# Optimization experiments

Hardware: AMD Instinct MI355X
Metric: run time of the kernel (lower is better)

Reference implementation:

```python
import jax, jax.numpy as jnp
import numpy as np

EPS_BN = 1e-5


def gcn_agg(h, src, dst, n):
    # remove_self_loops then add_self_loops, degree computed on dst (incl. self loops)
    valid = (src != dst).astype(h.dtype)  # mask out original self loops
    deg = jnp.zeros((n,), h.dtype).at[dst].add(valid) + 1.0  # +1 for added self loop
    dinv = deg ** -0.5
    w = dinv[src] * dinv[dst] * valid  # [E]
    # h_prime[dst] += w * h[src]; self-loop contributes deg^-1 * h
    out = jnp.zeros_like(h).at[dst].add(w[:, None] * h[src])
    out = out + (1.0 / deg)[:, None] * h
    return out


def batchnorm(h):
    # BatchNorm1d(affine=False, track_running_stats=False): batch stats, biased var
    mean = jnp.mean(h, axis=0)
    var = jnp.var(h, axis=0)
    return (h - mean) * jax.lax.rsqrt(var + EPS_BN)


def setup_inputs() -> dict:
    key = jax.random.key(0)
    ks = jax.random.split(key, 8)
    N, E, IN, HID, OUT = 50000, 640000, 500, 128, 64
    x = jax.random.normal(ks[0], (N, IN), jnp.float32)
    edge_index = jax.random.randint(ks[1], (2, E), 0, N, jnp.int64)
    def xavier(k, shape):
        gain = 1.414
        bound = gain * np.sqrt(6.0 / (shape[0] + shape[1]))
        return jax.random.uniform(k, shape, jnp.float32, -bound, bound)
    W0 = xavier(ks[2], (HID, IN))
    W1 = xavier(ks[3], (HID, HID))
    W2 = xavier(ks[4], (OUT, HID))
    b0 = jnp.zeros((HID,), jnp.float32)
    b1 = jnp.zeros((HID,), jnp.float32)
    b2 = jnp.zeros((OUT,), jnp.float32)
    return {"x": x, "edge_index": edge_index, "W0": W0, "b0": b0,
            "W1": W1, "b1": b1, "W2": W2, "b2": b2}


def reference(x, edge_index, W0, b0, W1, b1, W2, b2):
    n = x.shape[0]
    src, dst = edge_index[0], edge_index[1]
    # layer 0 and 1 (num_layers - 1 = 2), eval mode -> dropout is identity
    h = x @ W0.T
    h = gcn_agg(h, src, dst, n) + b0
    h = jax.nn.relu(batchnorm(h))
    h = h @ W1.T
    h = gcn_agg(h, src, dst, n) + b1
    h = jax.nn.relu(batchnorm(h))
    # classifier
    h = h @ W2.T
    h = gcn_agg(h, src, dst, n) + b2
    return jax.nn.log_softmax(h, axis=1)
```

## Files before the change

kernel.cpp:

```cpp
#include <hip/hip_runtime.h>
#include <hip/hip_bf16.h>
#include <math.h>


#define EPS_BN 1e-5f

typedef __attribute__((ext_vector_type(8))) _Float16 f16x8;
typedef __attribute__((ext_vector_type(4))) _Float16 f16x4;
typedef __attribute__((ext_vector_type(2))) _Float16 f16x2;
typedef __attribute__((ext_vector_type(4))) float    f32x4;

__device__ __forceinline__ void gload16(const void* g, void* l) {
    __builtin_amdgcn_global_load_lds(
        (const __attribute__((address_space(1))) void*)g,
        (__attribute__((address_space(3))) void*)l, 16, 0, 0);
}


__global__ void countw_k(const int* __restrict__ src, const int* __restrict__ dst,
                         int* __restrict__ cnt, int E, int gE,
                         const float* __restrict__ W0, _Float16* __restrict__ W0h,
                         const float* __restrict__ W1, _Float16* __restrict__ W1h,
                         const float* __restrict__ W2, _Float16* __restrict__ W2h) {
    if (blockIdx.x < (unsigned)gE) {
        int e = blockIdx.x * 256 + threadIdx.x;
        if (e >= E) return;
        int s = src[e], d = dst[e];
        if (s != d) atomicAdd(&cnt[d], 1);
        return;
    }
    int idx = (blockIdx.x - gE) * 256 + threadIdx.x;
    if (idx < 16384) {
        int r = idx >> 7, k4 = (idx & 127) * 4;
        f16x4 h = {(_Float16)0.f, (_Float16)0.f, (_Float16)0.f, (_Float16)0.f};
        if (k4 < 500) {
            float4 v = *(const float4*)(W0 + (size_t)r * 500 + k4);
            h[0] = (_Float16)v.x; h[1] = (_Float16)v.y;
            h[2] = (_Float16)v.z; h[3] = (_Float16)v.w;
        }
        *(f16x4*)(W0h + (size_t)r * 512 + k4) = h;
    } else if (idx < 16384 + 4096) {
        int t = idx - 16384;
        float4 v = *(const float4*)(W1 + (size_t)t * 4);
        f16x4 h;
        h[0] = (_Float16)v.x; h[1] = (_Float16)v.y;
        h[2] = (_Float16)v.z; h[3] = (_Float16)v.w;
        *(f16x4*)(W1h + (size_t)t * 4) = h;
    } else if (idx < 22528) {
        int t = idx - 20480;
        float4 v = *(const float4*)(W2 + (size_t)t * 4);
        f16x4 h;
        h[0] = (_Float16)v.x; h[1] = (_Float16)v.y;
        h[2] = (_Float16)v.z; h[3] = (_Float16)v.w;
        *(f16x4*)(W2h + (size_t)t * 4) = h;
    }
}

__global__ void scan1_k(const int* __restrict__ cnt, int* __restrict__ within,
                        int* __restrict__ btot, int n) {
    __shared__ int s[512];
    int tid = threadIdx.x;
    int i = blockIdx.x * 512 + tid;
    int val = (i < n) ? cnt[i] : 0;
    s[tid] = val;
    __syncthreads();
    for (int off = 1; off < 512; off <<= 1) {
        int v = (tid >= off) ? s[tid - off] : 0;
        __syncthreads();
        s[tid] += v;
        __syncthreads();
    }
    if (i < n) within[i] = s[tid] - val;
    if (tid == 511) btot[blockIdx.x] = s[511];
}

__global__ void scan3_k(const int* __restrict__ within, const int* __restrict__ btot,
                        const int* __restrict__ cnt, int* __restrict__ row_start,
                        int* __restrict__ cursor, float* __restrict__ dinv,
                        float* __restrict__ invdeg, int n) {
    __shared__ int sred[256];
    const int tid = threadIdx.x;
    const int w = (blockIdx.x * 256) >> 9;
    sred[tid] = (tid < w) ? btot[tid] : 0;
    __syncthreads();
    #pragma unroll
    for (int off = 128; off >= 1; off >>= 1) {
        if (tid < off) sred[tid] += sred[tid + off];
        __syncthreads();
    }
    const int base = sred[0];
    int i = blockIdx.x * 256 + tid;
    if (i < n) {
        int rs = within[i] + base;
        row_start[i] = rs;
        cursor[i]    = rs;
        float deg = (float)cnt[i] + 1.0f;
        dinv[i]   = rsqrtf(deg);
        invdeg[i] = 1.0f / deg;
    }
}


template <int NC, bool BN, bool AF32, bool FILL>
__global__ __launch_bounds__(256) void mgemm_k(const void* __restrict__ Av,
                                               const _Float16* __restrict__ Wh,
                                               _Float16* __restrict__ C,
                                               const float* __restrict__ gsum,
                                               const float* __restrict__ gsq,
                                               float inv_n, int M, int K, int Kp,
                                               const int* __restrict__ src,
                                               const int* __restrict__ dst,
                                               const float* __restrict__ dinv,
                                               int* __restrict__ cursor,
                                               int2* __restrict__ epk,
                                               int E, int gM) {
    constexpr int CT = NC / 16;
    constexpr int WJ = NC / 32;
    __shared__ __align__(16) _Float16 As[2][64 * 64];
    __shared__ __align__(16) _Float16 Ws[2][NC * 64];
    __shared__ __align__(16) float ssc[128], ssh[128];

    if constexpr (FILL) {
        if ((int)blockIdx.x >= gM) {
            int e = (blockIdx.x - gM) * 256 + threadIdx.x;
            if (e < E) {
                int s = src[e], d = dst[e];
                if (s != d) {
                    int pos = atomicAdd(&cursor[d], 1);
                    epk[pos] = make_int2(s, __float_as_int(dinv[s] * dinv[d]));
                }
            }
            return;
        }
    }

    const int tid  = threadIdx.x;
    const int lane = tid & 63, wave = tid >> 6;
    const int lrow = lane & 15, kg = lane >> 4;
    const int row0 = blockIdx.x * 64;

    f32x4 acc[CT] = {};
    float4 aw[4];

    const float*    Af = (const float*)Av;
    const _Float16* Ah = (const _Float16*)Av;

    auto stage = [&](int c0, int b) {
        const int k0 = c0 * 64;
        if constexpr (!AF32) {
            #pragma unroll
            for (int j = 0; j < 2; ++j) {
                int li  = wave * 128 + j * 64 + lane;
                int row = li >> 3, s = li & 7;
                int gr  = row0 + row;
                int gs  = s ^ (row & 7);
                if (gr < M)
                    gload16(Ah + (size_t)gr * Kp + k0 + gs * 8,
                            (char*)&As[b][0] + (wave * 128 + j * 64) * 16);
            }
        }
        #pragma unroll
        for (int j = 0; j < WJ; ++j) {
            int li  = wave * (WJ * 64) + j * 64 + lane;
            int row = li >> 3, s = li & 7;
            int gs  = s ^ (row & 7);
            gload16(Wh + (size_t)row * Kp + k0 + gs * 8,
                    (char*)&Ws[b][0] + (wave * WJ + j) * 1024);
        }
    };

    auto load_a = [&](int c0) {
        const int k0 = c0 * 64;
        #pragma unroll
        for (int it = 0; it < 4; ++it) {
            int idx = tid + it * 256;
            int row = idx >> 4, slot = idx & 15;
            int gr = row0 + row, gk = k0 + slot * 4;
            aw[it] = make_float4(0.f, 0.f, 0.f, 0.f);
            if (gr < M && gk < K)
                aw[it] = *(const float4*)(Af + (size_t)gr * K + gk);
        }
    };
    auto store_a = [&](int b) {
        #pragma unroll
        for (int it = 0; it < 4; ++it) {
            int idx = tid + it * 256;
            int row = idx >> 4, slot = idx & 15;
            f16x4 h;
            h[0] = (_Float16)aw[it].x; h[1] = (_Float16)aw[it].y;
            h[2] = (_Float16)aw[it].z; h[3] = (_Float16)aw[it].w;
            int cb = (slot * 8) ^ ((row & 7) << 4);
            *(f16x4*)((char*)&As[b][0] + row * 128 + cb) = h;
        }
    };

    auto compute = [&](int b, int kofs) {
        const char* AsB = (const char*)&As[b][0];
        const char* WsB = (const char*)&Ws[b][0];
        #pragma unroll
        for (int ks = 0; ks < 2; ++ks) {
            const int cbase = ks * 64 + kg * 16;
            f16x8 af, bf[CT];
            {
                int row = wave * 16 + lrow;
                af = *(const f16x8*)(AsB + row * 128 + (cbase ^ ((row & 7) << 4)));
            }
            if constexpr (BN) {
                const int kb = kofs + ks * 32 + kg * 8;
                f32x4 sc0 = *(const f32x4*)&ssc[kb];
                f32x4 sc1 = *(const f32x4*)&ssc[kb + 4];
                f32x4 sh0 = *(const f32x4*)&ssh[kb];
                f32x4 sh1 = *(const f32x4*)&ssh[kb + 4];
                f16x8 a2;
                #pragma unroll
                for (int j = 0; j < 4; ++j) {
                    a2[j]     = (_Float16)fmaxf(0.f, fmaf((float)af[j],     sc0[j], sh0[j]));
                    a2[j + 4] = (_Float16)fmaxf(0.f, fmaf((float)af[j + 4], sc1[j], sh1[j]));
                }
                af = a2;
            }
            #pragma unroll
            for (int ct = 0; ct < CT; ++ct) {
                int row = ct * 16 + lrow;
                bf[ct] = *(const f16x8*)(WsB + row * 128 + (cbase ^ ((row & 7) << 4)));
            }
            #pragma unroll
            for (int ct = 0; ct < CT; ++ct)
                acc[ct] = __builtin_amdgcn_mfma_f32_16x16x32_f16(
                    af, bf[ct], acc[ct], 0, 0, 0);
        }
    };

    if constexpr (BN) {
        if (tid < 128) {
            float mean = gsum[tid] * inv_n;
            float var  = gsq[tid] * inv_n - mean * mean;
            float sc   = rsqrtf(var + EPS_BN);
            ssc[tid] = sc;
            ssh[tid] = -mean * sc;
        }
    }

    const int nchunk = Kp >> 6;
    if constexpr (AF32) { load_a(0); }
    stage(0, 0);
    if constexpr (AF32) { store_a(0); }
    asm volatile("s_waitcnt vmcnt(0) lgkmcnt(0)" ::: "memory");
    __builtin_amdgcn_s_barrier();
    __builtin_amdgcn_sched_barrier(0);

    for (int c = 0; c < nchunk; ++c) {
        const int b = c & 1;
        const bool more = (c + 1 < nchunk);
        if (more) {
            stage(c + 1, b ^ 1);
            if constexpr (AF32) load_a(c + 1);
        }
        compute(b, c * 64);
        if (more) {
            if constexpr (AF32) store_a(b ^ 1);
            asm volatile("s_waitcnt vmcnt(0) lgkmcnt(0)" ::: "memory");
            __builtin_amdgcn_s_barrier();
            __builtin_amdgcn_sched_barrier(0);
        }
    }

    #pragma unroll
    for (int r = 0; r < 4; ++r) {
        int grow = row0 + wave * 16 + kg * 4 + r;
        if (grow >= M) continue;
        #pragma unroll
        for (int ct = 0; ct < CT; ++ct)
            C[(size_t)grow * NC + ct * 16 + lrow] = (_Float16)acc[ct][r];
    }
}


__global__ void agg128_k(const _Float16* __restrict__ h, const float* __restrict__ invdeg,
                         const int* __restrict__ row_start, const int* __restrict__ cnt,
                         const int2* __restrict__ epk,
                         const float* __restrict__ bias, _Float16* __restrict__ out, int n) {
    const int grp = threadIdx.x >> 4;
    const int l = threadIdx.x & 15;
    const int i = blockIdx.x * 16 + grp;
    if (i >= n) return;
    const int st = row_start[i], en = st + cnt[i];
    const float id = invdeg[i];
    const int c = l * 8;

    float a[8];
    {
        f16x8 hv = *(const f16x8*)(h + (size_t)i * 128 + c);
        #pragma unroll
        for (int j = 0; j < 8; ++j)
            a[j] = fmaf(id, (float)hv[j], bias[c + j]);
    }

    auto gfma = [&](int2 e0, int2 e1, int2 e2, int2 e3) {
        f16x8 v0 = *(const f16x8*)(h + (size_t)e0.x * 128 + c);
        f16x8 v1 = *(const f16x8*)(h + (size_t)e1.x * 128 + c);
        f16x8 v2 = *(const f16x8*)(h + (size_t)e2.x * 128 + c);
        f16x8 v3 = *(const f16x8*)(h + (size_t)e3.x * 128 + c);
        float w0 = __int_as_float(e0.y), w1 = __int_as_float(e1.y);
        float w2 = __int_as_float(e2.y), w3 = __int_as_float(e3.y);
        #pragma unroll
        for (int j = 0; j < 8; ++j) {
            a[j] = fmaf(w0, (float)v0[j], a[j]);
            a[j] = fmaf(w1, (float)v1[j], a[j]);
            a[j] = fmaf(w2, (float)v2[j], a[j]);
            a[j] = fmaf(w3, (float)v3[j], a[j]);
        }
    };

    int p = st;
    if (p + 3 < en) {
        int2 eA0 = epk[p], eA1 = epk[p + 1], eA2 = epk[p + 2], eA3 = epk[p + 3];
        while (p + 7 < en) {
            int2 eB0 = epk[p + 4], eB1 = epk[p + 5];
            int2 eB2 = epk[p + 6], eB3 = epk[p + 7];
            gfma(eA0, eA1, eA2, eA3);
            eA0 = eB0; eA1 = eB1; eA2 = eB2; eA3 = eB3;
            p += 4;
        }
        gfma(eA0, eA1, eA2, eA3);
        p += 4;
    }
    for (; p < en; ++p) {
        int2 e0 = epk[p];
        float w0 = __int_as_float(e0.y);
        f16x8 v0 = *(const f16x8*)(h + (size_t)e0.x * 128 + c);
        #pragma unroll
        for (int j = 0; j < 8; ++j)
            a[j] = fmaf(w0, (float)v0[j], a[j]);
    }
    f16x8 o;
    #pragma unroll
    for (int j = 0; j < 8; ++j) o[j] = (_Float16)a[j];
    *(f16x8*)(out + (size_t)i * 128 + c) = o;
}


__global__ void stats16_k(const _Float16* __restrict__ a, float* __restrict__ gsum,
                          float* __restrict__ gsq, int total8) {
    const int tid = threadIdx.x;
    float s[8] = {}, q[8] = {};
    for (int idx = blockIdx.x * 256 + tid; idx < total8; idx += gridDim.x * 256) {
        f16x8 v = *(const f16x8*)(a + (size_t)idx * 8);
        #pragma unroll
        for (int j = 0; j < 8; ++j) {
            float f = (float)v[j];
            s[j] += f;
            q[j] = fmaf(f, f, q[j]);
        }
    }
    __shared__ float red[2][16][16][8];
    const int g = tid & 15, k = tid >> 4;
    #pragma unroll
    for (int j = 0; j < 8; ++j) {
        red[0][k][g][j] = s[j];
        red[1][k][g][j] = q[j];
    }
    __syncthreads();
    if (tid < 128) {
        const int g2 = tid & 15, j2 = tid >> 4;
        float ts = 0.f, tq = 0.f;
        #pragma unroll
        for (int k2 = 0; k2 < 16; ++k2) {
            ts += red[0][k2][g2][j2];
            tq += red[1][k2][g2][j2];
        }
        atomicAdd(&gsum[g2 * 8 + j2], ts);
        atomicAdd(&gsq[g2 * 8 + j2], tq);
    }
}


__global__ void aggsm_k(const _Float16* __restrict__ h, const float* __restrict__ invdeg,
                        const int* __restrict__ row_start, const int* __restrict__ cnt,
                        const int2* __restrict__ epk,
                        const float* __restrict__ bias, float* __restrict__ out, int n) {
    const int grp = threadIdx.x >> 3;
    const int l = threadIdx.x & 7;
    const int i = blockIdx.x * 32 + grp;
    if (i >= n) return;
    const int st = row_start[i], en = st + cnt[i];
    const float id = invdeg[i];
    const int c = l * 8;

    float a[8];
    {
        f16x8 hv = *(const f16x8*)(h + (size_t)i * 64 + c);
        #pragma unroll
        for (int j = 0; j < 8; ++j)
            a[j] = fmaf(id, (float)hv[j], bias[c + j]);
    }

    auto gfma = [&](int2 e0, int2 e1, int2 e2, int2 e3) {
        f16x8 v0 = *(const f16x8*)(h + (size_t)e0.x * 64 + c);
        f16x8 v1 = *(const f16x8*)(h + (size_t)e1.x * 64 + c);
        f16x8 v2 = *(const f16x8*)(h + (size_t)e2.x * 64 + c);
        f16x8 v3 = *(const f16x8*)(h + (size_t)e3.x * 64 + c);
        float w0 = __int_as_float(e0.y), w1 = __int_as_float(e1.y);
        float w2 = __int_as_float(e2.y), w3 = __int_as_float(e3.y);
        #pragma unroll
        for (int j = 0; j < 8; ++j) {
            a[j] = fmaf(w0, (float)v0[j], a[j]);
            a[j] = fmaf(w1, (float)v1[j], a[j]);
            a[j] = fmaf(w2, (float)v2[j], a[j]);
            a[j] = fmaf(w3, (float)v3[j], a[j]);
        }
    };

    int p = st;
    if (p + 3 < en) {
        int2 eA0 = epk[p], eA1 = epk[p + 1], eA2 = epk[p + 2], eA3 = epk[p + 3];
        while (p + 7 < en) {
            int2 eB0 = epk[p + 4], eB1 = epk[p + 5];
            int2 eB2 = epk[p + 6], eB3 = epk[p + 7];
            gfma(eA0, eA1, eA2, eA3);
            eA0 = eB0; eA1 = eB1; eA2 = eB2; eA3 = eB3;
            p += 4;
        }
        gfma(eA0, eA1, eA2, eA3);
        p += 4;
    }
    for (; p < en; ++p) {
        int2 e0 = epk[p];
        float w0 = __int_as_float(e0.y);
        f16x8 v0 = *(const f16x8*)(h + (size_t)e0.x * 64 + c);
        #pragma unroll
        for (int j = 0; j < 8; ++j)
            a[j] = fmaf(w0, (float)v0[j], a[j]);
    }

    float m = a[0];
    #pragma unroll
    for (int j = 1; j < 8; ++j) m = fmaxf(m, a[j]);
    #pragma unroll
    for (int d = 4; d >= 1; d >>= 1) m = fmaxf(m, __shfl_xor(m, d, 64));
    float s = 0.f;
    float e[8];
    #pragma unroll
    for (int j = 0; j < 8; ++j) { e[j] = __expf(a[j] - m); s += e[j]; }
    #pragma unroll
    for (int d = 4; d >= 1; d >>= 1) s += __shfl_xor(s, d, 64);
    float ls = __logf(s);
    float4 o0 = make_float4(a[0] - m - ls, a[1] - m - ls,
                            a[2] - m - ls, a[3] - m - ls);
    float4 o1 = make_float4(a[4] - m - ls, a[5] - m - ls,
                            a[6] - m - ls, a[7] - m - ls);
    *(float4*)(out + (size_t)i * 64 + c)     = o0;
    *(float4*)(out + (size_t)i * 64 + c + 4) = o1;
}


extern "C" void kernel_launch(void* const* d_in, const int* in_sizes, int n_in,
                              void* d_out, int out_size, void* d_ws, size_t ws_size,
                              hipStream_t stream) {
    const float* x  = (const float*)d_in[0];
    const int*   ei = (const int*)d_in[1];
    const float* W0 = (const float*)d_in[2];
    const float* b0 = (const float*)d_in[3];
    const float* W1 = (const float*)d_in[4];
    const float* b1 = (const float*)d_in[5];
    const float* W2 = (const float*)d_in[6];
    const float* b2 = (const float*)d_in[7];

    const int IN = 500;
    const int n = in_sizes[0] / IN;
    const int E = in_sizes[1] / 2;
    const int* src = ei;
    const int* dst = ei + E;

    char* p = (char*)d_ws;
    auto alloc = [&](size_t bytes) -> void* {
        char* r = p;
        p += (bytes + 255) & ~(size_t)255;
        return (void*)r;
    };
    _Float16*  hb1h    = (_Float16*)alloc((size_t)n * 128 * 2);
    _Float16*  hb2a    = (_Float16*)alloc((size_t)n * 128 * 2);
    _Float16*  W0h     = (_Float16*)alloc((size_t)128 * 512 * 2);
    _Float16*  W1h     = (_Float16*)alloc((size_t)128 * 128 * 2);
    _Float16*  W2h     = (_Float16*)alloc((size_t)64 * 128 * 2);
    int*   deg_cnt  = (int*)alloc((size_t)n * 4);
    float* gsum0    = (float*)alloc(128 * 4);
    float* gsq0     = (float*)alloc(128 * 4);
    float* gsum1    = (float*)alloc(128 * 4);
    float* gsq1     = (float*)alloc(128 * 4);
    char*  zero_end = p;
    float* dinv     = (float*)alloc((size_t)n * 4);
    float* invdeg   = (float*)alloc((size_t)n * 4);
    int*   row_st   = (int*)alloc((size_t)n * 4);
    int*   cursor   = (int*)alloc((size_t)n * 4);
    int*   within   = (int*)alloc((size_t)n * 4);
    int*   btot     = (int*)alloc(256 * 4);
    int2*  epk      = (int2*)alloc((size_t)E * 8);
    (void)ws_size; (void)n_in; (void)out_size;

    float* out = (float*)d_out;
    const float inv_n = 1.0f / (float)n;

    const int gE = (E + 255) / 256;
    const int gN = (n + 255) / 256;
    const int nblk = (n + 511) / 512;
    const int gM = (n + 63) / 64;
    const int gA = (n + 15) / 16;
    const int gS = (n + 31) / 32;

    hipMemsetAsync(deg_cnt, 0, (size_t)(zero_end - (char*)deg_cnt), stream);
    countw_k<<<gE + 88, 256, 0, stream>>>(src, dst, deg_cnt, E, gE,
                                          W0, W0h, W1, W1h, W2, W2h);
    scan1_k<<<nblk, 512, 0, stream>>>(deg_cnt, within, btot, n);
    scan3_k<<<gN, 256, 0, stream>>>(within, btot, deg_cnt, row_st, cursor,
                                    dinv, invdeg, n);

    mgemm_k<128, false, true, true><<<gM + gE, 256, 0, stream>>>(
        x, W0h, hb1h, nullptr, nullptr, 0.f, n, 500, 512,
        src, dst, dinv, cursor, epk, E, gM);
    agg128_k<<<gA, 256, 0, stream>>>(hb1h, invdeg, row_st, deg_cnt, epk, b0, hb2a, n);
    stats16_k<<<256, 256, 0, stream>>>(hb2a, gsum0, gsq0, n * 16);

    mgemm_k<128, true, false, false><<<gM, 256, 0, stream>>>(
        hb2a, W1h, hb1h, gsum0, gsq0, inv_n, n, 128, 128,
        nullptr, nullptr, nullptr, nullptr, nullptr, 0, gM);
    agg128_k<<<gA, 256, 0, stream>>>(hb1h, invdeg, row_st, deg_cnt, epk, b1, hb2a, n);
    stats16_k<<<256, 256, 0, stream>>>(hb2a, gsum1, gsq1, n * 16);

    mgemm_k<64, true, false, false><<<gM, 256, 0, stream>>>(
        hb2a, W2h, hb1h, gsum1, gsq1, inv_n, n, 128, 128,
        nullptr, nullptr, nullptr, nullptr, nullptr, 0, gM);
    aggsm_k<<<gS, 256, 0, stream>>>(hb1h, invdeg, row_st, deg_cnt, epk, b2, out, n);
}
```

Before: 214.6 us.

## Prefetch fp32 A tiles two chunks ahead with register double-buffering

For the fp32-input GEMM path (the first layer's x @ W0ᵀ), A-tile global loads now go into two alternating register sets. Loads are issued two K-chunks ahead, and the barrier wait is relaxed to vmcnt(4) so the newest prefetch can stay in flight across the barrier. This hides global-load latency on the large fp32 input read. Out-of-range loads now use a clamped address and are zeroed afterwards instead of being branched around. The cost is more registers and a manually unrolled loop whose correctness depends on in-order vmcnt accounting. The fp16 path keeps the old schedule.

Measured after the change: 214.6 us, median of 4. Within noise of the previous version (-0.0%).

```diff
diff --git a/kernel.cpp b/kernel.cpp
--- a/kernel.cpp
+++ b/kernel.cpp
@@ -140,7 +140,8 @@
     const int row0 = blockIdx.x * 64;
 
     f32x4 acc[CT] = {};
-    float4 aw[4];
+    float4 awA0, awA1, awA2, awA3;
+    float4 awB0, awB1, awB2, awB3;
 
     const float*    Af = (const float*)Av;
     const _Float16* Ah = (const _Float16*)Av;
@@ -169,29 +170,41 @@
         }
     };
 
-    auto load_a = [&](int c0) {
-        const int k0 = c0 * 64;
-        #pragma unroll
-        for (int it = 0; it < 4; ++it) {
-            int idx = tid + it * 256;
-            int row = idx >> 4, slot = idx & 15;
-            int gr = row0 + row, gk = k0 + slot * 4;
-            aw[it] = make_float4(0.f, 0.f, 0.f, 0.f);
-            if (gr < M && gk < K)
-                aw[it] = *(const float4*)(Af + (size_t)gr * K + gk);
-        }
-    };
-    auto store_a = [&](int b) {
-        #pragma unroll
-        for (int it = 0; it < 4; ++it) {
-            int idx = tid + it * 256;
-            int row = idx >> 4, slot = idx & 15;
-            f16x4 h;
-            h[0] = (_Float16)aw[it].x; h[1] = (_Float16)aw[it].y;
-            h[2] = (_Float16)aw[it].z; h[3] = (_Float16)aw[it].w;
-            int cb = (slot * 8) ^ ((row & 7) << 4);
-            *(f16x4*)((char*)&As[b][0] + row * 128 + cb) = h;
-        }
+    auto load_one = [&](int c0, int it) -> float4 {
+        int idx = tid + it * 256;
+        int row = idx >> 4, slot = idx & 15;
+        int gr = row0 + row, gk = c0 * 64 + slot * 4;
+        bool ok = (gr < M) && (gk < K);
+        int grc = ok ? gr : 0;
+        int gkc = ok ? gk : 0;
+        float4 v = *(const float4*)(Af + (size_t)grc * K + gkc);
+        if (!ok) v = make_float4(0.f, 0.f, 0.f, 0.f);
+        return v;
+    };
+    auto load_aA = [&](int c0) {
+        awA0 = load_one(c0, 0); awA1 = load_one(c0, 1);
+        awA2 = load_one(c0, 2); awA3 = load_one(c0, 3);
+    };
+    auto load_aB = [&](int c0) {
+        awB0 = load_one(c0, 0); awB1 = load_one(c0, 1);
+        awB2 = load_one(c0, 2); awB3 = load_one(c0, 3);
+    };
+    auto store_one = [&](int b, int it, float4 v) {
+        int idx = tid + it * 256;
+        int row = idx >> 4, slot = idx & 15;
+        f16x4 h;
+        h[0] = (_Float16)v.x; h[1] = (_Float16)v.y;
+        h[2] = (_Float16)v.z; h[3] = (_Float16)v.w;
+        int cb = (slot * 8) ^ ((row & 7) << 4);
+        *(f16x4*)((char*)&As[b][0] + row * 128 + cb) = h;
+    };
+    auto store_aA = [&](int b) {
+        store_one(b, 0, awA0); store_one(b, 1, awA1);
+        store_one(b, 2, awA2); store_one(b, 3, awA3);
+    };
+    auto store_aB = [&](int b) {
+        store_one(b, 0, awB0); store_one(b, 1, awB1);
+        store_one(b, 2, awB2); store_one(b, 3, awB3);
     };
 
     auto compute = [&](int b, int kofs) {
@@ -242,26 +255,64 @@
     }
 
     const int nchunk = Kp >> 6;
-    if constexpr (AF32) { load_a(0); }
-    stage(0, 0);
-    if constexpr (AF32) { store_a(0); }
-    asm volatile("s_waitcnt vmcnt(0) lgkmcnt(0)" ::: "memory");
-    __builtin_amdgcn_s_barrier();
-    __builtin_amdgcn_sched_barrier(0);
-
-    for (int c = 0; c < nchunk; ++c) {
-        const int b = c & 1;
-        const bool more = (c + 1 < nchunk);
-        if (more) {
-            stage(c + 1, b ^ 1);
-            if constexpr (AF32) load_a(c + 1);
-        }
-        compute(b, c * 64);
-        if (more) {
-            if constexpr (AF32) store_a(b ^ 1);
-            asm volatile("s_waitcnt vmcnt(0) lgkmcnt(0)" ::: "memory");
-            __builtin_amdgcn_s_barrier();
-            __builtin_amdgcn_sched_barrier(0);
+
+    if constexpr (AF32) {
+        load_aA(0);
+        stage(0, 0);
+        load_aB(1);
+        store_aA(0);
+        asm volatile("s_waitcnt vmcnt(4) lgkmcnt(0)" ::: "memory");
+        __builtin_amdgcn_s_barrier();
+        __builtin_amdgcn_sched_barrier(0);
+
+        int c = 0;
+        while (true) {
+            {
+                const int b = c & 1;
+                const bool more = c + 1 < nchunk;
+                const bool pf   = c + 2 < nchunk;
+                if (more) stage(c + 1, b ^ 1);
+                if (pf)   load_aA(c + 2);
+                compute(b, 0);
+                if (!more) break;
+                store_aB(b ^ 1);
+                if (pf) asm volatile("s_waitcnt vmcnt(4) lgkmcnt(0)" ::: "memory");
+                else    asm volatile("s_waitcnt vmcnt(0) lgkmcnt(0)" ::: "memory");
+                __builtin_amdgcn_s_barrier();
+                __builtin_amdgcn_sched_barrier(0);
+                ++c;
+            }
+            {
+                const int b = c & 1;
+                const bool more = c + 1 < nchunk;
+                const bool pf   = c + 2 < nchunk;
+                if (more) stage(c + 1, b ^ 1);
+                if (pf)   load_aB(c + 2);
+                compute(b, 0);
+                if (!more) break;
+                store_aA(b ^ 1);
+                if (pf) asm volatile("s_waitcnt vmcnt(4) lgkmcnt(0)" ::: "memory");
+                else    asm volatile("s_waitcnt vmcnt(0) lgkmcnt(0)" ::: "memory");
+                __builtin_amdgcn_s_barrier();
+                __builtin_amdgcn_sched_barrier(0);
+                ++c;
+            }
+        }
+    } else {
+        stage(0, 0);
+        asm volatile("s_waitcnt vmcnt(0) lgkmcnt(0)" ::: "memory");
+        __builtin_amdgcn_s_barrier();
+        __builtin_amdgcn_sched_barrier(0);
+        for (int c = 0; c < nchunk; ++c) {
+            const int b = c & 1;
+            const bool more = (c + 1 < nchunk);
+            if (more) stage(c + 1, b ^ 1);
+            compute(b, c * 64);
+            if (more) {
+                asm volatile("s_waitcnt vmcnt(0) lgkmcnt(0)" ::: "memory");
+                __builtin_amdgcn_s_barrier();
+                __builtin_amdgcn_sched_barrier(0);
+            }
         }
     }
 
```

## Load whole fp32 A row-block into LDS upfront for first GEMM

Applied to the files above, without the earlier changes.

For the fp32-input GEMM (the 500-wide first layer), each wave now loads its 16 full rows of A once, converts them to fp16 and stores them in a 64x512 LDS tile before the K loop. The per-chunk register-staged load and store of A is removed, so each row is read with contiguous row-wide accesses and the loop only double-buffers W. This raises LDS use to about 64KB for A, which can lower occupancy, and the A global loads are no longer overlapped with compute.

Result: slower. 236.2 us (+10.1%).

```diff
diff --git a/kernel.cpp b/kernel.cpp
--- a/kernel.cpp
+++ b/kernel.cpp
@@ -116,7 +116,8 @@
                                                int E, int gM) {
     constexpr int CT = NC / 16;
     constexpr int WJ = NC / 32;
-    __shared__ __align__(16) _Float16 As[2][64 * 64];
+    constexpr int ASZ = AF32 ? (64 * 512) : (2 * 64 * 64);
+    __shared__ __align__(16) _Float16 As[ASZ];
     __shared__ __align__(16) _Float16 Ws[2][NC * 64];
     __shared__ __align__(16) float ssc[128], ssh[128];
 
@@ -140,7 +141,6 @@
     const int row0 = blockIdx.x * 64;
 
     f32x4 acc[CT] = {};
-    float4 aw[4];
 
     const float*    Af = (const float*)Av;
     const _Float16* Ah = (const _Float16*)Av;
@@ -156,7 +156,8 @@
                 int gs  = s ^ (row & 7);
                 if (gr < M)
                     gload16(Ah + (size_t)gr * Kp + k0 + gs * 8,
-                            (char*)&As[b][0] + (wave * 128 + j * 64) * 16);
+                            (char*)As + b * (64 * 64 * 2) +
+                            (wave * 128 + j * 64) * 16);
             }
         }
         #pragma unroll
@@ -169,41 +170,45 @@
         }
     };
 
-    auto load_a = [&](int c0) {
-        const int k0 = c0 * 64;
-        #pragma unroll
-        for (int it = 0; it < 4; ++it) {
-            int idx = tid + it * 256;
-            int row = idx >> 4, slot = idx & 15;
-            int gr = row0 + row, gk = k0 + slot * 4;
-            aw[it] = make_float4(0.f, 0.f, 0.f, 0.f);
-            if (gr < M && gk < K)
-                aw[it] = *(const float4*)(Af + (size_t)gr * K + gk);
+    auto fillA = [&]() {
+        #pragma unroll
+        for (int r = 0; r < 16; ++r) {
+            int row = wave * 16 + r;
+            int gr  = row0 + row;
+            if (gr >= M) continue;
+            const float* rowp = Af + (size_t)gr * K;
+            float4 v0 = *(const float4*)(rowp + lane * 4);
+            int s1 = 64 + lane;
+            float4 v1 = make_float4(0.f, 0.f, 0.f, 0.f);
+            if (s1 * 4 < K)
+                v1 = *(const float4*)(rowp + s1 * 4);
+            f16x4 h0, h1;
+            h0[0] = (_Float16)v0.x; h0[1] = (_Float16)v0.y;
+            h0[2] = (_Float16)v0.z; h0[3] = (_Float16)v0.w;
+            h1[0] = (_Float16)v1.x; h1[1] = (_Float16)v1.y;
+            h1[2] = (_Float16)v1.z; h1[3] = (_Float16)v1.w;
+            const int sw = (row & 7) << 4;
+            char* rb = (char*)As + row * 1024;
+            *(f16x4*)(rb + ((lane * 8) ^ sw)) = h0;
+            *(f16x4*)(rb + ((s1 * 8) ^ sw))  = h1;
         }
     };
-    auto store_a = [&](int b) {
-        #pragma unroll
-        for (int it = 0; it < 4; ++it) {
-            int idx = tid + it * 256;
-            int row = idx >> 4, slot = idx & 15;
-            f16x4 h;
-            h[0] = (_Float16)aw[it].x; h[1] = (_Float16)aw[it].y;
-            h[2] = (_Float16)aw[it].z; h[3] = (_Float16)aw[it].w;
-            int cb = (slot * 8) ^ ((row & 7) << 4);
-            *(f16x4*)((char*)&As[b][0] + row * 128 + cb) = h;
-        }
-    };
-
-    auto compute = [&](int b, int kofs) {
-        const char* AsB = (const char*)&As[b][0];
+
+    auto compute = [&](int b, int cchunk, int kofs) {
+        const char* AsB = (const char*)As + (AF32 ? 0 : b * (64 * 64 * 2));
         const char* WsB = (const char*)&Ws[b][0];
         #pragma unroll
         for (int ks = 0; ks < 2; ++ks) {
-            const int cbase = ks * 64 + kg * 16;
+            const int cb = ks * 64 + kg * 16;
             f16x8 af, bf[CT];
             {
                 int row = wave * 16 + lrow;
-                af = *(const f16x8*)(AsB + row * 128 + (cbase ^ ((row & 7) << 4)));
+                int sw  = (row & 7) << 4;
+                if constexpr (AF32)
+                    af = *(const f16x8*)(AsB + row * 1024 +
+                                         ((cchunk * 128 + cb) ^ sw));
+                else
+                    af = *(const f16x8*)(AsB + row * 128 + (cb ^ sw));
             }
             if constexpr (BN) {
                 const int kb = kofs + ks * 32 + kg * 8;
@@ -222,7 +227,8 @@
             #pragma unroll
             for (int ct = 0; ct < CT; ++ct) {
                 int row = ct * 16 + lrow;
-                bf[ct] = *(const f16x8*)(WsB + row * 128 + (cbase ^ ((row & 7) << 4)));
+                bf[ct] = *(const f16x8*)(WsB + row * 128 +
+                                         (cb ^ ((row & 7) << 4)));
             }
             #pragma unroll
             for (int ct = 0; ct < CT; ++ct)
@@ -242,26 +248,39 @@
     }
 
     const int nchunk = Kp >> 6;
-    if constexpr (AF32) { load_a(0); }
-    stage(0, 0);
-    if constexpr (AF32) { store_a(0); }
-    asm volatile("s_waitcnt vmcnt(0) lgkmcnt(0)" ::: "memory");
-    __builtin_amdgcn_s_barrier();
-    __builtin_amdgcn_sched_barrier(0);
-
-    for (int c = 0; c < nchunk; ++c) {
-        const int b = c & 1;
-        const bool more = (c + 1 < nchunk);
-        if (more) {
-            stage(c + 1, b ^ 1);
-            if constexpr (AF32) load_a(c + 1);
-        }
-        compute(b, c * 64);
-        if (more) {
-            if constexpr (AF32) store_a(b ^ 1);
-            asm volatile("s_waitcnt vmcnt(0) lgkmcnt(0)" ::: "memory");
-            __builtin_amdgcn_s_barrier();
-            __builtin_amdgcn_sched_barrier(0);
+
+    if constexpr (AF32) {
+        fillA();
+        stage(0, 0);
+        asm volatile("s_waitcnt vmcnt(0) lgkmcnt(0)" ::: "memory");
+        __builtin_amdgcn_s_barrier();
+        __builtin_amdgcn_sched_barrier(0);
+        for (int c = 0; c < nchunk; ++c) {
+            const int b = c & 1;
+            const bool more = (c + 1 < nchunk);
+            if (more) stage(c + 1, b ^ 1);
+            compute(b, c, 0);
+            if (more) {
+                asm volatile("s_waitcnt vmcnt(0)" ::: "memory");
+                __builtin_amdgcn_s_barrier();
+                __builtin_amdgcn_sched_barrier(0);
+            }
+        }
+    } else {
+        stage(0, 0);
+        asm volatile("s_waitcnt vmcnt(0) lgkmcnt(0)" ::: "memory");
+        __builtin_amdgcn_s_barrier();
+        __builtin_amdgcn_sched_barrier(0);
+        for (int c = 0; c < nchunk; ++c) {
+            const int b = c & 1;
+            const bool more = (c + 1 < nchunk);
+            if (more) stage(c + 1, b ^ 1);
+            compute(b, c, c * 64);
+            if (more) {
+                asm volatile("s_waitcnt vmcnt(0) lgkmcnt(0)" ::: "memory");
+                __builtin_amdgcn_s_barrier();
+                __builtin_amdgcn_sched_barrier(0);
+            }
         }
     }
 
```
